# Kernel tuning notes

Measured on AMD Instinct MI355X. Metric: run time of the kernel, lower is better.

## Reference

```python
import jax, jax.numpy as jnp
import numpy as np

ALPHA = -10.0  # softmax sharpness on |x - bin| distances
TAU = 0.0
TAU2 = 0.0
EPS = 1e-10

B, F, L, K = 32, 64, 1024, 32


def setup_inputs() -> dict:
    key = jax.random.key(0)
    k1, k2 = jax.random.split(key)
    x = jax.random.normal(k1, (B, F, L), dtype=jnp.float32)
    bins = jax.random.normal(k2, (K,), dtype=jnp.float32)
    return {"x": x, "bins": bins}


def reference(x, bins):
    # dist: [B, F, L, K] = |x[..., None] - bins|
    dist = jnp.abs(x[..., None] - bins)
    # soft assignment over the K bins (training path of the module)
    soft = jax.nn.softmax(ALPHA * dist, axis=-1)
    assignment = soft + EPS

    # weighted quantization loss: sum of per-bin mean of sqrt(assignment)
    quant = jnp.sum(jnp.mean(jnp.sqrt(assignment), axis=(0, 1, 2)))
    weighted_quant_loss = jnp.stack([quant, jnp.float32(TAU2)])[None, :]  # [1, 2]

    # code entropy of average assignment distribution
    p = jnp.mean(assignment, axis=(0, 1, 2))  # [K]
    code_entropy = -jnp.sum(p * jnp.log(p))
    weighted_code_entropy = jnp.stack([code_entropy, jnp.float32(TAU)])[None, :]  # [1, 2]

    # soft reconstruction against the bins: [B, F, L]
    bit_code = jnp.einsum('bflk,k->bfl', assignment, bins)
    return bit_code, weighted_code_entropy, weighted_quant_loss
```

## Files before the change

### kernel.cpp

```cpp
#include <hip/hip_runtime.h>

#define K      32
#define KH     16
#define TPB    256
#define NB     2048
#define EPT    8
#define NTOT   (32 * 64 * 1024)
#define PSTRIDE (NB * (TPB / 2))

__device__ __forceinline__ float wave_reduce_sum(float v) {
#pragma unroll
  for (int m = 1; m < 64; m <<= 1) v += __shfl_xor(v, m, 64);
  return v;
}

__device__ __forceinline__ float pair_lane_reduce(float v) {
#pragma unroll
  for (int m = 2; m < 64; m <<= 1) v += __shfl_xor(v, m, 64);
  return v;
}

__global__ __launch_bounds__(TPB)
void ssq_main(const float* __restrict__ x, const float* __restrict__ bins,
              float* __restrict__ out, float* __restrict__ partials) {
  const int tid  = threadIdx.x;
  const int half = tid & 1;
  const int pslot = blockIdx.x * (TPB / 2) + (tid >> 1);

  float binv[KH];
#pragma unroll
  for (int j = 0; j < KH; ++j) binv[j] = bins[KH * half + j];
  float bs_local = 0.f;
#pragma unroll
  for (int j = 0; j < KH; ++j) bs_local += binv[j];
  const float binsum = bs_local + __shfl_xor(bs_local, 1, 64);
  const float epsb = 1e-10f * binsum;

  float xs[EPT];
#pragma unroll
  for (int e = 0; e < EPT; ++e) xs[e] = x[pslot + e * PSTRIDE];

  float sAcc[KH];
#pragma unroll
  for (int j = 0; j < KH; ++j) sAcc[j] = 0.f;
  float q = 0.f;

  const float Ch = -7.213475204444817f;

#pragma unroll 1
  for (int e = 0; e < EPT; ++e) {
    const float xv = xs[e];
    float t[KH];
    float s0 = 0.f, s1 = 0.f, h0 = 0.f, h1 = 0.f, b0 = 0.f, b1 = 0.f;
#pragma unroll
    for (int j = 0; j < KH; j += 2) {
      float ha = __builtin_amdgcn_exp2f(Ch * fabsf(xv - binv[j + 0]));
      float hb = __builtin_amdgcn_exp2f(Ch * fabsf(xv - binv[j + 1]));
      float ta = ha * ha, tb = hb * hb;
      t[j + 0] = ta; t[j + 1] = tb;
      s0 += ta; s1 += tb;
      h0 += ha; h1 += hb;
      b0 = fmaf(ta, binv[j + 0], b0);
      b1 = fmaf(tb, binv[j + 1], b1);
    }
    const float s_loc = s0 + s1;
    const float b_loc = b0 + b1;
    const float s_full = s_loc + __shfl_xor(s_loc, 1, 64);
    const float b_full = b_loc + __shfl_xor(b_loc, 1, 64);
    const float inv = __builtin_amdgcn_rcpf(s_full);
    q = fmaf(h0 + h1, __builtin_amdgcn_rsqf(s_full), q);
    if (half == 0) out[pslot + e * PSTRIDE] = fmaf(b_full, inv, epsb);
#pragma unroll
    for (int j = 0; j < KH; ++j) sAcc[j] = fmaf(t[j], inv, sAcc[j]);
  }

  __shared__ float red[4][K + 1];
  const int lane = tid & 63, wv = tid >> 6;
#pragma unroll
  for (int j = 0; j < KH; ++j) {
    float v = pair_lane_reduce(sAcc[j]);
    if (lane < 2) red[wv][KH * lane + j] = v;
  }
  {
    float v = wave_reduce_sum(q);
    if (lane == 0) red[wv][K] = v;
  }
  __syncthreads();
  if (tid < K + 1) {
    float v = red[0][tid] + red[1][tid] + red[2][tid] + red[3][tid];
    partials[tid * NB + blockIdx.x] = v;
  }
}

__global__ __launch_bounds__(TPB)
void ssq_reduce(const float* __restrict__ partials, float* __restrict__ sums) {
  const float* p = partials + blockIdx.x * NB;
  const int tid  = threadIdx.x;
  float s = 0.f;
#pragma unroll
  for (int j = 0; j < NB / TPB; ++j) s += p[tid + j * TPB];
  s = wave_reduce_sum(s);
  __shared__ float red[4];
  if ((tid & 63) == 0) red[tid >> 6] = s;
  __syncthreads();
  if (tid == 0) sums[blockIdx.x] = red[0] + red[1] + red[2] + red[3];
}

__global__ void ssq_final(const float* __restrict__ sums, float* __restrict__ out) {
  const int lane = threadIdx.x;
  float e = 0.f;
  if (lane < K) {
    float p = sums[lane] * (1.0f / (float)NTOT) + 1e-10f;
    e = -p * __logf(p);
  }
  e = wave_reduce_sum(e);
  if (lane == 0) {
    out[NTOT + 0] = e;
    out[NTOT + 1] = 0.f;
    out[NTOT + 2] = sums[K] * (1.0f / (float)NTOT);
    out[NTOT + 3] = 0.f;
  }
}

extern "C" void kernel_launch(void* const* d_in, const int* in_sizes, int n_in,
                              void* d_out, int out_size, void* d_ws, size_t ws_size,
                              hipStream_t stream) {
  const float* x    = (const float*)d_in[0];
  const float* bins = (const float*)d_in[1];
  float* out        = (float*)d_out;
  float* partials   = (float*)d_ws;
  float* sums       = partials + (K + 1) * NB;

  ssq_main  <<<NB,    TPB, 0, stream>>>(x, bins, out, partials);
  ssq_reduce<<<K + 1, TPB, 0, stream>>>(partials, sums);
  ssq_final <<<1,     64,  0, stream>>>(sums, out);
}
```

Measured before the change: 84.10 us.

## Split bins across four lanes per element and merge reduction kernels

Each element's 32 bins are now handled by four lanes of 8 bins each instead of two lanes of 16, so twice as many blocks are launched and each thread needs fewer registers. Per-element sums are combined with an extra shuffle step. The separate partial-reduce and final-entropy kernels are merged into one 1024-thread block, which removes one kernel launch. The trade-off is more shuffles per element, partials that are twice as large, and a single-block tail reduction with less parallelism.

```diff
diff --git a/kernel.cpp b/kernel.cpp
--- a/kernel.cpp
+++ b/kernel.cpp
@@ -1,12 +1,12 @@
 #include <hip/hip_runtime.h>
 
 #define K      32
-#define KH     16
+#define KQ     8
 #define TPB    256
-#define NB     2048
+#define NB     4096
 #define EPT    8
 #define NTOT   (32 * 64 * 1024)
-#define PSTRIDE (NB * (TPB / 2))
+#define PSTRIDE (NB * (TPB / 4))
 
 __device__ __forceinline__ float wave_reduce_sum(float v) {
 #pragma unroll
@@ -14,35 +14,36 @@
   return v;
 }
 
-__device__ __forceinline__ float pair_lane_reduce(float v) {
+__device__ __forceinline__ float quarter_reduce(float v) {
 #pragma unroll
-  for (int m = 2; m < 64; m <<= 1) v += __shfl_xor(v, m, 64);
+  for (int m = 4; m < 64; m <<= 1) v += __shfl_xor(v, m, 64);
   return v;
 }
 
 __global__ __launch_bounds__(TPB)
 void ssq_main(const float* __restrict__ x, const float* __restrict__ bins,
               float* __restrict__ out, float* __restrict__ partials) {
-  const int tid  = threadIdx.x;
-  const int half = tid & 1;
-  const int pslot = blockIdx.x * (TPB / 2) + (tid >> 1);
+  const int tid     = threadIdx.x;
+  const int quarter = tid & 3;
+  const int pslot   = blockIdx.x * (TPB / 4) + (tid >> 2);
 
-  float binv[KH];
+  float binv[KQ];
 #pragma unroll
-  for (int j = 0; j < KH; ++j) binv[j] = bins[KH * half + j];
-  float bs_local = 0.f;
+  for (int j = 0; j < KQ; ++j) binv[j] = bins[KQ * quarter + j];
+  float bs = 0.f;
 #pragma unroll
-  for (int j = 0; j < KH; ++j) bs_local += binv[j];
-  const float binsum = bs_local + __shfl_xor(bs_local, 1, 64);
-  const float epsb = 1e-10f * binsum;
+  for (int j = 0; j < KQ; ++j) bs += binv[j];
+  bs += __shfl_xor(bs, 1, 64);
+  bs += __shfl_xor(bs, 2, 64);
+  const float epsb = 1e-10f * bs;
 
   float xs[EPT];
 #pragma unroll
   for (int e = 0; e < EPT; ++e) xs[e] = x[pslot + e * PSTRIDE];
 
-  float sAcc[KH];
+  float sAcc[KQ];
 #pragma unroll
-  for (int j = 0; j < KH; ++j) sAcc[j] = 0.f;
+  for (int j = 0; j < KQ; ++j) sAcc[j] = 0.f;
   float q = 0.f;
 
   const float Ch = -7.213475204444817f;
@@ -50,10 +51,10 @@
 #pragma unroll 1
   for (int e = 0; e < EPT; ++e) {
     const float xv = xs[e];
-    float t[KH];
+    float t[KQ];
     float s0 = 0.f, s1 = 0.f, h0 = 0.f, h1 = 0.f, b0 = 0.f, b1 = 0.f;
 #pragma unroll
-    for (int j = 0; j < KH; j += 2) {
+    for (int j = 0; j < KQ; j += 2) {
       float ha = __builtin_amdgcn_exp2f(Ch * fabsf(xv - binv[j + 0]));
       float hb = __builtin_amdgcn_exp2f(Ch * fabsf(xv - binv[j + 1]));
       float ta = ha * ha, tb = hb * hb;
@@ -63,23 +64,24 @@
       b0 = fmaf(ta, binv[j + 0], b0);
       b1 = fmaf(tb, binv[j + 1], b1);
     }
-    const float s_loc = s0 + s1;
-    const float b_loc = b0 + b1;
-    const float s_full = s_loc + __shfl_xor(s_loc, 1, 64);
-    const float b_full = b_loc + __shfl_xor(b_loc, 1, 64);
+    float s_loc = s0 + s1, b_loc = b0 + b1;
+    float s2 = s_loc + __shfl_xor(s_loc, 1, 64);
+    float b2 = b_loc + __shfl_xor(b_loc, 1, 64);
+    const float s_full = s2 + __shfl_xor(s2, 2, 64);
+    const float b_full = b2 + __shfl_xor(b2, 2, 64);
     const float inv = __builtin_amdgcn_rcpf(s_full);
     q = fmaf(h0 + h1, __builtin_amdgcn_rsqf(s_full), q);
-    if (half == 0) out[pslot + e * PSTRIDE] = fmaf(b_full, inv, epsb);
+    if (quarter == 0) out[pslot + e * PSTRIDE] = fmaf(b_full, inv, epsb);
 #pragma unroll
-    for (int j = 0; j < KH; ++j) sAcc[j] = fmaf(t[j], inv, sAcc[j]);
+    for (int j = 0; j < KQ; ++j) sAcc[j] = fmaf(t[j], inv, sAcc[j]);
   }
 
   __shared__ float red[4][K + 1];
   const int lane = tid & 63, wv = tid >> 6;
 #pragma unroll
-  for (int j = 0; j < KH; ++j) {
-    float v = pair_lane_reduce(sAcc[j]);
-    if (lane < 2) red[wv][KH * lane + j] = v;
+  for (int j = 0; j < KQ; ++j) {
+    float v = quarter_reduce(sAcc[j]);
+    if (lane < 4) red[wv][KQ * lane + j] = v;
   }
   {
     float v = wave_reduce_sum(q);
@@ -92,33 +94,32 @@
   }
 }
 
-__global__ __launch_bounds__(TPB)
-void ssq_reduce(const float* __restrict__ partials, float* __restrict__ sums) {
-  const float* p = partials + blockIdx.x * NB;
-  const int tid  = threadIdx.x;
-  float s = 0.f;
+__global__ __launch_bounds__(1024)
+void ssq_tail(const float* __restrict__ partials, float* __restrict__ out) {
+  const int tid = threadIdx.x, lane = tid & 63, wv = tid >> 6;
+  __shared__ float sums[K + 1];
+  for (int c = wv; c < K + 1; c += 16) {
+    const float* p = partials + c * NB;
+    float s = 0.f;
 #pragma unroll
-  for (int j = 0; j < NB / TPB; ++j) s += p[tid + j * TPB];
-  s = wave_reduce_sum(s);
-  __shared__ float red[4];
-  if ((tid & 63) == 0) red[tid >> 6] = s;
+    for (int j = 0; j < NB / 64; ++j) s += p[lane + j * 64];
+    s = wave_reduce_sum(s);
+    if (lane == 0) sums[c] = s;
+  }
   __syncthreads();
-  if (tid == 0) sums[blockIdx.x] = red[0] + red[1] + red[2] + red[3];
-}
-
-__global__ void ssq_final(const float* __restrict__ sums, float* __restrict__ out) {
-  const int lane = threadIdx.x;
-  float e = 0.f;
-  if (lane < K) {
-    float p = sums[lane] * (1.0f / (float)NTOT) + 1e-10f;
-    e = -p * __logf(p);
-  }
-  e = wave_reduce_sum(e);
-  if (lane == 0) {
-    out[NTOT + 0] = e;
-    out[NTOT + 1] = 0.f;
-    out[NTOT + 2] = sums[K] * (1.0f / (float)NTOT);
-    out[NTOT + 3] = 0.f;
+  if (wv == 0) {
+    float e = 0.f;
+    if (lane < K) {
+      float p = sums[lane] * (1.0f / (float)NTOT) + 1e-10f;
+      e = -p * __logf(p);
+    }
+    e = wave_reduce_sum(e);
+    if (lane == 0) {
+      out[NTOT + 0] = e;
+      out[NTOT + 1] = 0.f;
+      out[NTOT + 2] = sums[K] * (1.0f / (float)NTOT);
+      out[NTOT + 3] = 0.f;
+    }
   }
 }
 
@@ -129,9 +130,7 @@
   const float* bins = (const float*)d_in[1];
   float* out        = (float*)d_out;
   float* partials   = (float*)d_ws;
-  float* sums       = partials + (K + 1) * NB;
 
-  ssq_main  <<<NB,    TPB, 0, stream>>>(x, bins, out, partials);
-  ssq_reduce<<<K + 1, TPB, 0, stream>>>(partials, sums);
-  ssq_final <<<1,     64,  0, stream>>>(sums, out);
+  ssq_main<<<NB, TPB,  0, stream>>>(x, bins, out, partials);
+  ssq_tail<<<1,  1024, 0, stream>>>(partials, out);
 }
```

Result: slower. 87.46 us (+4.0%).

## Factor exp of absolute distance into precomputed per-bin and per-element exponentials

Applied to the files above, without the earlier changes.

Replaces the per-bin exp2 of |x-b| with the minimum of two products of precomputed exponentials: per-bin factors are computed once and only four exp2 per element remain. The half-sharpness term used for the sqrt loss is handled the same way. Pair-lane shuffles are replaced by DPP quad-permute moves. This cuts transcendental throughput pressure but raises register use and risks overflow or precision loss for inputs far from the bins.

```diff
diff --git a/kernel.cpp b/kernel.cpp
--- a/kernel.cpp
+++ b/kernel.cpp
@@ -13,28 +13,41 @@
   for (int m = 1; m < 64; m <<= 1) v += __shfl_xor(v, m, 64);
   return v;
 }
-
 __device__ __forceinline__ float pair_lane_reduce(float v) {
 #pragma unroll
   for (int m = 2; m < 64; m <<= 1) v += __shfl_xor(v, m, 64);
   return v;
 }
+__device__ __forceinline__ float dpp_xor1(float v) {
+  return __int_as_float(__builtin_amdgcn_update_dpp(
+      0, __float_as_int(v), 0xB1, 0xF, 0xF, true));
+}
 
 __global__ __launch_bounds__(TPB)
 void ssq_main(const float* __restrict__ x, const float* __restrict__ bins,
               float* __restrict__ out, float* __restrict__ partials) {
-  const int tid  = threadIdx.x;
-  const int half = tid & 1;
+  const int tid   = threadIdx.x;
+  const int half  = tid & 1;
   const int pslot = blockIdx.x * (TPB / 2) + (tid >> 1);
 
-  float binv[KH];
+  const float Cf = -14.426950408889634f;
+
+  float bl[KH], iz[KH], ez[KH], ihz[KH], ehz[KH];
 #pragma unroll
-  for (int j = 0; j < KH; ++j) binv[j] = bins[KH * half + j];
-  float bs_local = 0.f;
+  for (int j = 0; j < KH; ++j) {
+    float b = bins[KH * half + j];
+    float z = Cf * b;
+    bl[j]  = b;
+    iz[j]  = __builtin_amdgcn_exp2f(-z);
+    ez[j]  = __builtin_amdgcn_exp2f(z);
+    ihz[j] = __builtin_amdgcn_exp2f(-0.5f * z);
+    ehz[j] = __builtin_amdgcn_exp2f(0.5f * z);
+  }
+  float bs = 0.f;
 #pragma unroll
-  for (int j = 0; j < KH; ++j) bs_local += binv[j];
-  const float binsum = bs_local + __shfl_xor(bs_local, 1, 64);
-  const float epsb = 1e-10f * binsum;
+  for (int j = 0; j < KH; ++j) bs += bl[j];
+  bs += dpp_xor1(bs);
+  const float epsb = 1e-10f * bs;
 
   float xs[EPT];
 #pragma unroll
@@ -45,28 +58,33 @@
   for (int j = 0; j < KH; ++j) sAcc[j] = 0.f;
   float q = 0.f;
 
-  const float Ch = -7.213475204444817f;
-
 #pragma unroll 1
   for (int e = 0; e < EPT; ++e) {
     const float xv = xs[e];
+    const float y  = Cf * xv;
+    const float Ey  = __builtin_amdgcn_exp2f(y);
+    const float iEy = __builtin_amdgcn_exp2f(-y);
+    const float Eh  = __builtin_amdgcn_exp2f(0.5f * y);
+    const float iEh = __builtin_amdgcn_exp2f(-0.5f * y);
     float t[KH];
     float s0 = 0.f, s1 = 0.f, h0 = 0.f, h1 = 0.f, b0 = 0.f, b1 = 0.f;
 #pragma unroll
     for (int j = 0; j < KH; j += 2) {
-      float ha = __builtin_amdgcn_exp2f(Ch * fabsf(xv - binv[j + 0]));
-      float hb = __builtin_amdgcn_exp2f(Ch * fabsf(xv - binv[j + 1]));
-      float ta = ha * ha, tb = hb * hb;
+      float pa = Ey * iz[j + 0], ma = iEy * ez[j + 0];
+      float pb = Ey * iz[j + 1], mb = iEy * ez[j + 1];
+      float ta = fminf(pa, ma), tb = fminf(pb, mb);
       t[j + 0] = ta; t[j + 1] = tb;
       s0 += ta; s1 += tb;
-      h0 += ha; h1 += hb;
-      b0 = fmaf(ta, binv[j + 0], b0);
-      b1 = fmaf(tb, binv[j + 1], b1);
+      b0 = fmaf(ta, bl[j + 0], b0);
+      b1 = fmaf(tb, bl[j + 1], b1);
+      float hpa = Eh * ihz[j + 0], hma = iEh * ehz[j + 0];
+      float hpb = Eh * ihz[j + 1], hmb = iEh * ehz[j + 1];
+      h0 += fminf(hpa, hma);
+      h1 += fminf(hpb, hmb);
     }
-    const float s_loc = s0 + s1;
-    const float b_loc = b0 + b1;
-    const float s_full = s_loc + __shfl_xor(s_loc, 1, 64);
-    const float b_full = b_loc + __shfl_xor(b_loc, 1, 64);
+    float s_loc = s0 + s1, b_loc = b0 + b1;
+    const float s_full = s_loc + dpp_xor1(s_loc);
+    const float b_full = b_loc + dpp_xor1(b_loc);
     const float inv = __builtin_amdgcn_rcpf(s_full);
     q = fmaf(h0 + h1, __builtin_amdgcn_rsqf(s_full), q);
     if (half == 0) out[pslot + e * PSTRIDE] = fmaf(b_full, inv, epsb);
```

Result: slower. 89.93 us (+6.9%).
